# Optimization experiments

Measured on AMD Instinct MI355X. Metric: run time of the kernel, lower is better.

Reference implementation:

```python
import jax, jax.numpy as jnp
import numpy as np

INV_L_MIN, INV_L_MAX = 0.5, 2.0

def _gelu(v):
    return jax.nn.gelu(v, approximate=False)  # torch F.gelu default = exact erf

def compute_gradient(f, directed_edges, edge_gradient_weights):
    # f: [b, c, n] ; directed_edges: [b, e, 2] (target, source) ; egw: [b, e, d]
    f = jnp.transpose(f, (0, 2, 1))                      # [b, n, c]
    b, n, c = f.shape
    e, d = edge_gradient_weights.shape[1], edge_gradient_weights.shape[2]
    target, source = directed_edges[..., 0], directed_edges[..., 1]
    fs = jnp.take_along_axis(f, source[:, :, None], axis=1)   # [b, e, c]
    ft = jnp.take_along_axis(f, target[:, :, None], axis=1)   # [b, e, c]
    # einsum('bed,bec->becd') then reshape -> channel-major (c*d) layout
    msg = (edge_gradient_weights[:, :, None, :] * (fs - ft)[:, :, :, None]).reshape(b, e, c * d)
    seg = (target + n * jnp.arange(b, dtype=target.dtype)[:, None]).reshape(-1)
    grad = jax.ops.segment_sum(msg.reshape(b * e, c * d), seg, num_segments=b * n)
    return jnp.transpose(grad.reshape(b, n, c * d), (0, 2, 1))  # [b, c*d, n]

def spectral_conv(x, wc, ws_, w0, bc, bs, b0, wbc, wbs, wb0):
    # x: [b, c, n]; bases: [b, n, k, w]; weights: [c, o, k, w]
    xc = jnp.einsum('bcx,bxkw->bckw', x, wbc)
    xs = jnp.einsum('bcx,bxkw->bckw', x, wbs)
    x0 = jnp.einsum('bcx,bxkw->bckw', x, wb0)
    fc = jnp.einsum('bckw,cokw->bokw', xc, wc) - jnp.einsum('bckw,cokw->bokw', xs, ws_)
    fs = jnp.einsum('bckw,cokw->bokw', xs, wc) + jnp.einsum('bckw,cokw->bokw', xc, ws_)
    f0 = jnp.einsum('bckw,cokw->bokw', x0, w0)
    return (jnp.einsum('bokw,bxkw->box', f0, b0)
            + 2 * jnp.einsum('bokw,bxkw->box', fc, bc)
            - 2 * jnp.einsum('bokw,bxkw->box', fs, bs))

def setup_inputs():
    key = jax.random.key(0)
    ks = jax.random.split(key, 16)
    B, N, E = 4, 20000, 100000
    NDIMS, NMEAS, NMODES = 3, 1, 32
    C, L = 128, 3
    IN_DIM, FC_DIM, OUT_DIM = 3, 128, 1
    f32 = jnp.float32
    inp = {}
    inp['x'] = jax.random.normal(ks[0], (B, N, IN_DIM), f32)
    inp['node_mask'] = jnp.ones((B, N, 1), jnp.int32)
    inp['nodes'] = jax.random.uniform(ks[1], (B, N, NDIMS), f32)
    inp['node_weights'] = jax.random.uniform(ks[2], (B, N, NMEAS), f32) / N
    inp['directed_edges'] = jax.random.randint(ks[3], (B, E, 2), 0, N, jnp.int32)
    inp['edge_gradient_weights'] = jax.random.normal(ks[4], (B, E, NDIMS), f32)
    # modes k = 2*pi*K/L0, K integer-like
    inp['modes'] = (2 * jnp.pi * jax.random.randint(ks[5], (NMODES, NDIMS, NMEAS), 1, 9)).astype(f32)
    # scaled_logit(1.0, 0.5, 2.0): sigmoid(l)=1/3 -> l=log(0.5)
    inp['inv_L_scale_latent'] = jnp.full((NDIMS, NMEAS), np.log(0.5), f32)
    inp['fc0_w'] = jax.random.normal(ks[6], (C, IN_DIM), f32) / np.sqrt(IN_DIM)
    inp['fc0_b'] = jnp.zeros((C,), f32)
    sc = 1.0 / (C * C)
    inp['swc'] = sc * jax.random.uniform(ks[7], (L, C, C, NMODES, NMEAS), f32)
    inp['sws'] = sc * jax.random.uniform(ks[8], (L, C, C, NMODES, NMEAS), f32)
    inp['sw0'] = sc * jax.random.uniform(ks[9], (L, C, C, 1, NMEAS), f32)
    inp['ww'] = jax.random.normal(ks[10], (L, C, C), f32) / np.sqrt(C)
    inp['wb'] = jnp.zeros((L, C), f32)
    inp['gw'] = jax.random.normal(ks[11], (L, C, NDIMS * C), f32) / np.sqrt(NDIMS * C)
    inp['gb'] = jnp.zeros((L, C), f32)
    inp['fc1_w'] = jax.random.normal(ks[12], (FC_DIM, C), f32) / np.sqrt(C)
    inp['fc1_b'] = jnp.zeros((FC_DIM,), f32)
    inp['fc2_w'] = jax.random.normal(ks[13], (OUT_DIM, FC_DIM), f32) / np.sqrt(FC_DIM)
    inp['fc2_b'] = jnp.zeros((OUT_DIM,), f32)
    return inp

def reference(x, node_mask, nodes, node_weights, directed_edges, edge_gradient_weights,
              modes, inv_L_scale_latent, fc0_w, fc0_b, swc, sws, sw0, ww, wb, gw, gb,
              fc1_w, fc1_b, fc2_w, fc2_b):
    inv_L = INV_L_MIN + (INV_L_MAX - INV_L_MIN) * jax.nn.sigmoid(inv_L_scale_latent)  # [d, w]
    t = jnp.einsum('bxd,kdw->bxkw', nodes, modes * inv_L[None])
    bc, bs = jnp.cos(t), jnp.sin(t)
    b0 = jnp.ones(t.shape[:2] + (1, t.shape[3]), t.dtype)
    w = node_weights[:, :, None, :]
    wbc, wbs, wb0 = bc * w, bs * w, b0 * w
    h = jnp.einsum('bni,ci->bnc', x, fc0_w) + fc0_b        # lift
    h = jnp.transpose(h, (0, 2, 1))                        # [b, C, n]
    L = swc.shape[0]
    for i in range(L):
        h1 = spectral_conv(h, swc[i], sws[i], sw0[i], bc, bs, b0, wbc, wbs, wb0)
        h2 = jnp.einsum('oc,bcn->bon', ww[i], h) + wb[i][None, :, None]
        g = compute_gradient(h, directed_edges, edge_gradient_weights)
        h3 = jnp.einsum('oc,bcn->bon', gw[i], g) + gb[i][None, :, None]
        h = h1 + h2 + h3
        if i != L - 1:
            h = _gelu(h)
    h = jnp.transpose(h, (0, 2, 1))                        # [b, n, C]
    h = _gelu(h @ fc1_w.T + fc1_b)
    return h @ fc2_w.T + fc2_b                             # [b, n, out_dim]
```

## Files before the change

kernel.cpp:

```cpp
#include <hip/hip_runtime.h>
#include <math.h>

#define B_ 4
#define N_ 20000
#define E_ 100000
#define C_ 128
#define K_ 32
#define NPAD 20480
#define NROWS (B_*N_ + 128)

typedef __attribute__((ext_vector_type(8))) short short8;
typedef __attribute__((ext_vector_type(4))) float floatx4;
typedef __attribute__((ext_vector_type(4))) unsigned int uintx4;
typedef __attribute__((ext_vector_type(2))) unsigned int uintx2;

__device__ __forceinline__ float gelu_exact(float x){
    return 0.5f * x * (1.0f + erff(x * 0.70710678118654752f));
}

__device__ __forceinline__ unsigned short f2bf(float f){
    unsigned int u = __builtin_bit_cast(unsigned int, f);
    u += 0x7FFFu + ((u >> 16) & 1u);
    return (unsigned short)(u >> 16);
}
__device__ __forceinline__ unsigned int pack2(float a, float b){
    return (unsigned int)f2bf(a) | ((unsigned int)f2bf(b) << 16);
}
__device__ __forceinline__ float bf2f(unsigned short u){
    unsigned int v = ((unsigned int)u) << 16;
    return __builtin_bit_cast(float, v);
}
__device__ __forceinline__ float u2f(unsigned int u){
    return __builtin_bit_cast(float, u);
}


__global__ __launch_bounds__(256) void basis_kernel(
    const float* __restrict__ nodes, const float* __restrict__ nw,
    const float* __restrict__ modes, const float* __restrict__ latent,
    unsigned short* __restrict__ bcb, unsigned short* __restrict__ bsb,
    unsigned short* __restrict__ wBt)
{
    __shared__ float lx[64], ly[64], lz[64], lwv[64];
    __shared__ unsigned short lTc[32*64], lTs[32*64];
    int b = blockIdx.y, n0 = blockIdx.x*64;
    int tid = threadIdx.x;
    size_t bN = (size_t)b*N_;
    if (tid < 64){
        int n = n0 + tid;
        float iL0 = 0.5f + 1.5f/(1.f+expf(-latent[0]));
        float iL1 = 0.5f + 1.5f/(1.f+expf(-latent[1]));
        float iL2 = 0.5f + 1.5f/(1.f+expf(-latent[2]));
        if (n < N_){
            lx[tid] = nodes[(bN+n)*3+0]*iL0;
            ly[tid] = nodes[(bN+n)*3+1]*iL1;
            lz[tid] = nodes[(bN+n)*3+2]*iL2;
            lwv[tid] = nw[bN+n];
        } else { lx[tid]=0.f; ly[tid]=0.f; lz[tid]=0.f; lwv[tid]=0.f; }
    }
    __syncthreads();
    int node = tid>>2, k0 = (tid&3)*8;
    float p0 = lx[node], p1 = ly[node], p2 = lz[node], w = lwv[node];
    float cv[8], sv[8];
    #pragma unroll
    for (int i=0;i<8;i++){
        int k = k0+i;
        float t = p0*modes[k*3+0] + p1*modes[k*3+1] + p2*modes[k*3+2];
        cv[i] = cosf(t); sv[i] = sinf(t);
        lTc[k*64 + node] = f2bf(w*cv[i]);
        lTs[k*64 + node] = f2bf(w*sv[i]);
    }
    int gn = n0 + node;
    if (gn < N_){
        uintx4 uc = (uintx4){pack2(cv[0],cv[1]), pack2(cv[2],cv[3]),
                             pack2(cv[4],cv[5]), pack2(cv[6],cv[7])};
        uintx4 us = (uintx4){pack2(sv[0],sv[1]), pack2(sv[2],sv[3]),
                             pack2(sv[4],sv[5]), pack2(sv[6],sv[7])};
        *(uintx4*)&bcb[(bN+gn)*K_ + k0] = uc;
        *(uintx4*)&bsb[(bN+gn)*K_ + k0] = us;
    }
    __syncthreads();
    #pragma unroll
    for (int i=0;i<5;i++){
        int idx = i*256 + tid;
        int row = idx>>4, seg = idx&15;
        unsigned short v0,v1,v2,v3;
        if (row < 32){
            v0=lTc[row*64+seg*4+0]; v1=lTc[row*64+seg*4+1];
            v2=lTc[row*64+seg*4+2]; v3=lTc[row*64+seg*4+3];
        } else if (row < 64){
            int r = row-32;
            v0=lTs[r*64+seg*4+0]; v1=lTs[r*64+seg*4+1];
            v2=lTs[r*64+seg*4+2]; v3=lTs[r*64+seg*4+3];
        } else if (row == 64){
            v0=f2bf(lwv[seg*4+0]); v1=f2bf(lwv[seg*4+1]);
            v2=f2bf(lwv[seg*4+2]); v3=f2bf(lwv[seg*4+3]);
        } else { v0=v1=v2=v3=0; }
        uintx2 u;
        u.x = (unsigned int)v0 | ((unsigned int)v1<<16);
        u.y = (unsigned int)v2 | ((unsigned int)v3<<16);
        *(uintx2*)&wBt[((size_t)b*80+row)*NPAD + n0 + seg*4] = u;
    }
}


__global__ __launch_bounds__(256) void fc0_kernel(
    const float* __restrict__ x, const float* __restrict__ w,
    const float* __restrict__ bvec, unsigned short* __restrict__ hN,
    unsigned short* __restrict__ hT)
{
    int idx = blockIdx.x*256 + threadIdx.x;
    if (idx >= B_*N_) return;
    int b = idx / N_, n = idx - b*N_;
    float x0 = x[(size_t)idx*3+0], x1 = x[(size_t)idx*3+1], x2 = x[(size_t)idx*3+2];
    unsigned short* hr = hN + (size_t)idx*C_;
    for (int c=0;c<C_;c+=4){
        float4 v;
        v.x = bvec[c+0] + x0*w[(c+0)*3] + x1*w[(c+0)*3+1] + x2*w[(c+0)*3+2];
        v.y = bvec[c+1] + x0*w[(c+1)*3] + x1*w[(c+1)*3+1] + x2*w[(c+1)*3+2];
        v.z = bvec[c+2] + x0*w[(c+2)*3] + x1*w[(c+2)*3+1] + x2*w[(c+2)*3+2];
        v.w = bvec[c+3] + x0*w[(c+3)*3] + x1*w[(c+3)*3+1] + x2*w[(c+3)*3+2];
        uintx2 u; u.x = pack2(v.x,v.y); u.y = pack2(v.z,v.w);
        *(uintx2*)(hr+c) = u;
        hT[((size_t)b*C_+c+0)*NPAD + n] = f2bf(v.x);
        hT[((size_t)b*C_+c+1)*NPAD + n] = f2bf(v.y);
        hT[((size_t)b*C_+c+2)*NPAD + n] = f2bf(v.z);
        hT[((size_t)b*C_+c+3)*NPAD + n] = f2bf(v.w);
    }
}


__global__ __launch_bounds__(256) void hist_kernel(
    const int* __restrict__ edges, int* __restrict__ cnt)
{
    int idx = blockIdx.x*256 + threadIdx.x;
    if (idx >= B_*E_) return;
    int b = idx / E_;
    int t = edges[(size_t)idx*2];
    atomicAdd(cnt + b*N_ + t, 1);
}

__global__ __launch_bounds__(1024) void scan_kernel(
    const int* __restrict__ cnt, int* __restrict__ rowptr, int* __restrict__ cur)
{
    __shared__ int wsum[16];
    int b = blockIdx.x, tid = threadIdx.x;
    int lane = tid & 63, wv = tid >> 6;
    const int CHUNK = 20;
    int start = tid * CHUNK;
    int lc[CHUNK];
    int lsum = 0;
    #pragma unroll
    for (int i=0;i<CHUNK;i++){
        int n = start + i;
        int v = (n < N_) ? cnt[b*N_+n] : 0;
        lc[i] = v; lsum += v;
    }
    int v = lsum;
    #pragma unroll
    for (int off=1; off<64; off<<=1){
        int t = __shfl_up(v, off, 64);
        if (lane >= off) v += t;
    }
    if (lane == 63) wsum[wv] = v;
    __syncthreads();
    if (wv == 0 && lane < 16){
        int wv2 = wsum[lane];
        #pragma unroll
        for (int off=1; off<16; off<<=1){
            int t = __shfl_up(wv2, off, 64);
            if (lane >= off) wv2 += t;
        }
        wsum[lane] = wv2;
    }
    __syncthreads();
    int waveoff = (wv == 0) ? 0 : wsum[wv-1];
    int excl = waveoff + v - lsum;
    #pragma unroll
    for (int i=0;i<CHUNK;i++){
        int n = start + i;
        if (n < N_){
            rowptr[b*(N_+1)+n] = excl;
            cur[b*N_+n] = excl;
            excl += lc[i];
        }
    }
    if (tid == 0) rowptr[b*(N_+1)+N_] = E_;
}

__global__ __launch_bounds__(256) void fill_kernel(
    const int* __restrict__ edges, const float* __restrict__ egw,
    int* __restrict__ cur, uintx4* __restrict__ epack)
{
    int idx = blockIdx.x*256 + threadIdx.x;
    if (idx >= B_*E_) return;
    int b = idx / E_;
    int t = edges[(size_t)idx*2];
    int src = edges[(size_t)idx*2+1];
    uintx4 rec;
    rec.x = (unsigned int)src;
    rec.y = __builtin_bit_cast(unsigned int, egw[(size_t)idx*3+0]);
    rec.z = __builtin_bit_cast(unsigned int, egw[(size_t)idx*3+1]);
    rec.w = __builtin_bit_cast(unsigned int, egw[(size_t)idx*3+2]);
    int pos = atomicAdd(cur + b*N_ + t, 1);
    epack[(size_t)b*E_ + pos] = rec;
}


__global__ __launch_bounds__(256) void wconv_kernel(
    const float* __restrict__ ww, const float* __restrict__ gw,
    unsigned short* __restrict__ wcat3)
{
    int o = blockIdx.x, l = blockIdx.y, t = threadIdx.x;
    const float* ww_l = ww + (size_t)l*C_*C_;
    const float* gw_l = gw + (size_t)l*C_*C_*3;
    int k = t*2;
    float a, bv;
    if (k < 128){ a = ww_l[(size_t)o*C_ + k];      bv = ww_l[(size_t)o*C_ + k + 1]; }
    else        { a = gw_l[(size_t)o*384 + k-128]; bv = gw_l[(size_t)o*384 + k-127]; }
    *(unsigned int*)&wcat3[((size_t)l*C_ + o)*512 + k] = pack2(a, bv);
}

__global__ __launch_bounds__(64) void fc1conv_kernel(
    const float* __restrict__ fc1w, unsigned short* __restrict__ w16)
{
    int o = blockIdx.x, t = threadIdx.x;
    int k = t*2;
    *(unsigned int*)&w16[(size_t)o*C_ + k] = pack2(fc1w[(size_t)o*C_+k], fc1w[(size_t)o*C_+k+1]);
}


__global__ __launch_bounds__(256) void stageA_kernel(
    const unsigned short* __restrict__ hT, const unsigned short* __restrict__ wBt,
    float* __restrict__ part)
{
    __shared__ unsigned short As[80*72];
    __shared__ unsigned short Bs[128*72];
    int b = blockIdx.y, blk = blockIdx.x;
    int tid = threadIdx.x;
    int wv = tid>>6, lane = tid&63, l15 = lane&15, quad = lane>>4;
    floatx4 acc[5][2];
    #pragma unroll
    for (int mt=0;mt<5;mt++){ acc[mt][0]=(floatx4){0,0,0,0}; acc[mt][1]=(floatx4){0,0,0,0}; }
    size_t hbase = (size_t)b*C_*NPAD;
    size_t wbase = (size_t)b*80*NPAD;
    for (int cidx=0; cidx<5; ++cidx){
        int n0c = blk*320 + cidx*64;
        #pragma unroll
        for (int i=0;i<3;i++){
            int idx = i*256 + tid;
            if (idx < 640){
                int row = idx>>3, seg = idx&7;
                uintx4 v = *(const uintx4*)&wBt[wbase + (size_t)row*NPAD + n0c + seg*8];
                *(uintx4*)&As[row*72 + seg*8] = v;
            }
        }
        #pragma unroll
        for (int i=0;i<4;i++){
            int idx = i*256 + tid;
            int row = idx>>3, seg = idx&7;
            int node = n0c + seg*8;
            uintx4 v = (uintx4){0,0,0,0};
            if (node < N_)
                v = *(const uintx4*)&hT[hbase + (size_t)row*NPAD + node];
            *(uintx4*)&Bs[row*72 + seg*8] = v;
        }
        __syncthreads();
        #pragma unroll
        for (int ks=0; ks<2; ks++){
            short8 bfrag[2];
            #pragma unroll
            for (int ot=0;ot<2;ot++)
                bfrag[ot] = *(const short8*)&Bs[(wv*32+ot*16+l15)*72 + ks*32 + quad*8];
            #pragma unroll
            for (int mt=0;mt<5;mt++){
                short8 af = *(const short8*)&As[(mt*16+l15)*72 + ks*32 + quad*8];
                acc[mt][0] = __builtin_amdgcn_mfma_f32_16x16x32_bf16(af, bfrag[0], acc[mt][0], 0,0,0);
                acc[mt][1] = __builtin_amdgcn_mfma_f32_16x16x32_bf16(af, bfrag[1], acc[mt][1], 0,0,0);
            }
        }
        __syncthreads();
    }
    float* pblk = part + ((size_t)(b*64+blk))*80*C_;
    #pragma unroll
    for (int mt=0;mt<5;mt++){
        #pragma unroll
        for (int ot=0;ot<2;ot++){
            int c = wv*32 + ot*16 + l15;
            #pragma unroll
            for (int r=0;r<4;r++){
                int kcol = mt*16 + quad*4 + r;
                pblk[kcol*C_ + c] = acc[mt][ot][r];
            }
        }
    }
}

__global__ __launch_bounds__(256) void reducePart_kernel(
    const float* __restrict__ part, float* __restrict__ xq)
{
    int idx = blockIdx.x*256 + threadIdx.x;
    if (idx >= B_*80*C_) return;
    int b = idx / (80*C_);
    int r = idx - b*80*C_;
    float s = 0.f;
    for (int blk=0; blk<64; blk++)
        s += part[((size_t)(b*64+blk))*80*C_ + r];
    xq[idx] = s;
}


__global__ __launch_bounds__(256) void mix_kernel(
    const float* __restrict__ xq, const float* __restrict__ swc_l,
    const float* __restrict__ sws_l, const float* __restrict__ sw0_l,
    unsigned short* __restrict__ wfb, float* __restrict__ f0)
{
    __shared__ float s64[4][64];
    int o = blockIdx.x, tid = threadIdx.x;
    int b = tid >> 6, t = tid & 63;
    int k = t & 31; bool isS = t >= 32;
    const float* xqb = xq + (size_t)b*80*C_;
    float acc = 0.f;
    for (int c=0;c<C_;c++){
        float xc = xqb[k*C_ + c], xs = xqb[(32+k)*C_ + c];
        float wc = swc_l[((size_t)c*C_+o)*K_ + k];
        float ws = sws_l[((size_t)c*C_+o)*K_ + k];
        acc += isS ? (xs*wc + xc*ws) : (xc*wc - xs*ws);
    }
    wfb[((size_t)b*C_+o)*64 + t] = f2bf(isS ? -2.f*acc : 2.f*acc);
    float p = xqb[64*C_ + t]      * sw0_l[(size_t)t*C_+o]
            + xqb[64*C_ + 64 + t] * sw0_l[(size_t)(t+64)*C_+o];
    s64[b][t] = p; __syncthreads();
    if (t==0){
        float s=0.f;
        for (int i=0;i<64;i++) s += s64[b][i];
        f0[b*C_+o] = s;
    }
}


__global__ __launch_bounds__(256) void grad_kernel(
    const unsigned short* __restrict__ hN, const uintx4* __restrict__ epack,
    const int* __restrict__ rowptr, unsigned short* __restrict__ g)
{
    int flat = blockIdx.x;
    int xcd = flat & 7;
    int b = xcd >> 1;
    int grp = (flat >> 3)*2 + (xcd & 1);
    int n = grp*4 + (threadIdx.x >> 6);
    int cp = threadIdx.x & 63;
    size_t bN = (size_t)b*N_;
    size_t bE = (size_t)b*E_;
    int r0 = rowptr[b*(N_+1)+n], r1 = rowptr[b*(N_+1)+n+1];
    unsigned int hcu = *(const unsigned int*)&hN[(bN+n)*C_ + cp*2];
    float hc0 = bf2f((unsigned short)hcu), hc1 = bf2f((unsigned short)(hcu>>16));
    float a00=0.f,a01=0.f,a02=0.f, a10=0.f,a11=0.f,a12=0.f;
    int i = r0;
    for (; i + 1 < r1; i += 2){
        uintx4 p0 = epack[bE + i];
        uintx4 p1 = epack[bE + i + 1];
        int s0 = (int)p0.x, s1 = (int)p1.x;
        unsigned int u0 = *(const unsigned int*)&hN[(bN+s0)*C_ + cp*2];
        unsigned int u1 = *(const unsigned int*)&hN[(bN+s1)*C_ + cp*2];
        float w00 = u2f(p0.y), w01 = u2f(p0.z), w02 = u2f(p0.w);
        float w10 = u2f(p1.y), w11 = u2f(p1.z), w12 = u2f(p1.w);
        float d00 = bf2f((unsigned short)u0) - hc0;
        float d01 = bf2f((unsigned short)(u0>>16)) - hc1;
        float d10 = bf2f((unsigned short)u1) - hc0;
        float d11 = bf2f((unsigned short)(u1>>16)) - hc1;
        a00 += w00*d00; a01 += w01*d00; a02 += w02*d00;
        a10 += w00*d01; a11 += w01*d01; a12 += w02*d01;
        a00 += w10*d10; a01 += w11*d10; a02 += w12*d10;
        a10 += w10*d11; a11 += w11*d11; a12 += w12*d11;
    }
    if (i < r1){
        uintx4 p0 = epack[bE + i];
        int s0 = (int)p0.x;
        unsigned int u0 = *(const unsigned int*)&hN[(bN+s0)*C_ + cp*2];
        float w00 = u2f(p0.y), w01 = u2f(p0.z), w02 = u2f(p0.w);
        float d00 = bf2f((unsigned short)u0) - hc0;
        float d01 = bf2f((unsigned short)(u0>>16)) - hc1;
        a00 += w00*d00; a01 += w01*d00; a02 += w02*d00;
        a10 += w00*d01; a11 += w01*d01; a12 += w02*d01;
    }
    unsigned short* gr = g + (bN+n)*(size_t)384 + cp*6;
    *(unsigned int*)(gr+0) = pack2(a00,a01);
    *(unsigned int*)(gr+2) = pack2(a02,a10);
    *(unsigned int*)(gr+4) = pack2(a11,a12);
}


__global__ __launch_bounds__(256) void gemm_kernel(
    const unsigned short* __restrict__ hN, const unsigned short* __restrict__ g,
    const unsigned short* __restrict__ bcb, const unsigned short* __restrict__ bsb,
    const unsigned short* __restrict__ wcat, const unsigned short* __restrict__ wfb,
    const float* __restrict__ wb_l, const float* __restrict__ gb_l,
    const float* __restrict__ f0,
    unsigned short* __restrict__ hNo, unsigned short* __restrict__ hT, int apply_gelu)
{
    __shared__ unsigned short As[2][64*72];
    int b = blockIdx.y;
    int nb0 = blockIdx.x*64;
    int tid = threadIdx.x;
    int a_n = tid>>2, a_s = tid&3;
    int wv = tid>>6, lane = tid&63, l15 = lane&15, quad = lane>>4;
    floatx4 acc[4][2];
    #pragma unroll
    for (int mt=0;mt<4;mt++)
        #pragma unroll
        for (int ot=0;ot<2;ot++) acc[mt][ot] = (floatx4){0.f,0.f,0.f,0.f};
    size_t bN = (size_t)b*N_;
    int gn = nb0 + a_n; bool av = gn < N_;
    size_t row = bN + (size_t)(av ? gn : 0);
    const unsigned short* hrow  = hN + row*C_;
    const unsigned short* grow  = g  + row*384;
    const unsigned short* bcrow = bcb + row*K_;
    const unsigned short* bsrow = bsb + row*K_;
    int o0 = wv*32 + l15, o1 = o0 + 16;
    const unsigned short* w0p = wcat + (size_t)o0*512 + quad*8;
    const unsigned short* w1p = wcat + (size_t)o1*512 + quad*8;
    const unsigned short* fb0 = wfb + ((size_t)b*C_ + o0)*64 + quad*8;
    const unsigned short* fb1 = wfb + ((size_t)b*C_ + o1)*64 + quad*8;

    auto loadA = [&](int ch, uintx4& v0, uintx4& v1){
        v0 = (uintx4){0,0,0,0}; v1 = (uintx4){0,0,0,0};
        if (av){
            if (ch < 8){
                const uintx4* p = (ch<2) ? (const uintx4*)(hrow + ch*64 + a_s*16)
                                         : (const uintx4*)(grow + (ch-2)*64 + a_s*16);
                v0 = p[0]; v1 = p[1];
            } else {
                const uintx4* p = (a_s < 2) ? (const uintx4*)(bcrow + a_s*16)
                                            : (const uintx4*)(bsrow + (a_s-2)*16);
                v0 = p[0]; v1 = p[1];
            }
        }
    };

    uintx4 c0, c1;
    loadA(0, c0, c1);
    *(uintx4*)&As[0][a_n*72 + a_s*16]     = c0;
    *(uintx4*)&As[0][a_n*72 + a_s*16 + 8] = c1;
    int p = 0;
    for (int ch=0; ch<9; ++ch){
        uintx4 n0v, n1v;
        if (ch < 8) loadA(ch+1, n0v, n1v);
        __syncthreads();
        #pragma unroll
        for (int ks=0; ks<2; ks++){
            short8 bfr0, bfr1;
            if (ch < 8){
                bfr0 = *(const short8*)(w0p + ch*64 + ks*32);
                bfr1 = *(const short8*)(w1p + ch*64 + ks*32);
            } else {
                bfr0 = *(const short8*)(fb0 + ks*32);
                bfr1 = *(const short8*)(fb1 + ks*32);
            }
            #pragma unroll
            for (int mt=0; mt<4; mt++){
                short8 af = *(const short8*)&As[p][(mt*16+l15)*72 + ks*32 + quad*8];
                acc[mt][0] = __builtin_amdgcn_mfma_f32_16x16x32_bf16(af, bfr0, acc[mt][0], 0,0,0);
                acc[mt][1] = __builtin_amdgcn_mfma_f32_16x16x32_bf16(af, bfr1, acc[mt][1], 0,0,0);
            }
        }
        if (ch < 8){
            *(uintx4*)&As[1-p][a_n*72 + a_s*16]     = n0v;
            *(uintx4*)&As[1-p][a_n*72 + a_s*16 + 8] = n1v;
            p ^= 1;
        }
    }
    float biasv[2]; int oo[2];
    oo[0]=o0; oo[1]=o1;
    #pragma unroll
    for (int ot=0;ot<2;ot++)
        biasv[ot] = wb_l[oo[ot]] + gb_l[oo[ot]] + f0[(size_t)b*C_ + oo[ot]];
    unsigned short* AsF = &As[0][0];
    if (apply_gelu) __syncthreads();
    #pragma unroll
    for (int mt=0;mt<4;mt++){
        #pragma unroll
        for (int ot=0;ot<2;ot++){
            int nb = nb0 + mt*16 + quad*4;
            float v4[4];
            #pragma unroll
            for (int r=0;r<4;r++){
                float vv = acc[mt][ot][r] + biasv[ot];
                if (apply_gelu) vv = gelu_exact(vv);
                v4[r] = vv;
                if (nb + r < N_) hNo[(bN+nb+r)*C_ + oo[ot]] = f2bf(vv);
            }
            if (apply_gelu){
                uintx2 u; u.x = pack2(v4[0],v4[1]); u.y = pack2(v4[2],v4[3]);
                *(uintx2*)&AsF[oo[ot]*72 + mt*16 + quad*4] = u;
            }
        }
    }
    if (apply_gelu){
        __syncthreads();
        int orow = tid>>1, half = tid&1;
        uintx4 u0 = *(const uintx4*)&AsF[orow*72 + half*32];
        uintx4 u1 = *(const uintx4*)&AsF[orow*72 + half*32 + 8];
        unsigned short* dst = &hT[((size_t)b*C_ + orow)*NPAD + nb0 + half*32];
        *(uintx4*)dst       = u0;
        *(uintx4*)(dst + 8) = u1;
    }
}


__global__ __launch_bounds__(256) void final_kernel(
    const unsigned short* __restrict__ hN, const unsigned short* __restrict__ fc1b16,
    const float* __restrict__ fc1b, const float* __restrict__ fc2w,
    const float* __restrict__ fc2b, float* __restrict__ out)
{
    __shared__ unsigned short As[64*72];
    __shared__ float pp[4*64];
    int b = blockIdx.y;
    int nb0 = blockIdx.x*64;
    int tid = threadIdx.x;
    int a_n = tid>>2, a_s = tid&3;
    int wv = tid>>6, lane = tid&63, l15 = lane&15, quad = lane>>4;
    floatx4 acc[4][2];
    #pragma unroll
    for (int mt=0;mt<4;mt++){ acc[mt][0]=(floatx4){0,0,0,0}; acc[mt][1]=(floatx4){0,0,0,0}; }
    size_t bN = (size_t)b*N_;
    int gn = nb0 + a_n; bool av = gn < N_;
    size_t row = bN + (size_t)(av ? gn : 0);
    const unsigned short* hrow = hN + row*C_;
    int o0 = wv*32 + l15, o1 = o0 + 16;
    const unsigned short* w0p = fc1b16 + (size_t)o0*C_ + quad*8;
    const unsigned short* w1p = fc1b16 + (size_t)o1*C_ + quad*8;

    for (int ch=0; ch<2; ++ch){
        uintx4 v0 = (uintx4){0,0,0,0}, v1 = (uintx4){0,0,0,0};
        if (av){
            const uintx4* pptr = (const uintx4*)(hrow + ch*64 + a_s*16);
            v0 = pptr[0]; v1 = pptr[1];
        }
        *(uintx4*)&As[a_n*72 + a_s*16]     = v0;
        *(uintx4*)&As[a_n*72 + a_s*16 + 8] = v1;
        __syncthreads();
        #pragma unroll
        for (int ks=0; ks<2; ks++){
            short8 bfr0 = *(const short8*)(w0p + ch*64 + ks*32);
            short8 bfr1 = *(const short8*)(w1p + ch*64 + ks*32);
            #pragma unroll
            for (int mt=0; mt<4; mt++){
                short8 af = *(const short8*)&As[(mt*16+l15)*72 + ks*32 + quad*8];
                acc[mt][0] = __builtin_amdgcn_mfma_f32_16x16x32_bf16(af, bfr0, acc[mt][0], 0,0,0);
                acc[mt][1] = __builtin_amdgcn_mfma_f32_16x16x32_bf16(af, bfr1, acc[mt][1], 0,0,0);
            }
        }
        __syncthreads();
    }
    float fw0 = fc2w[o0], fw1 = fc2w[o1];
    float b0 = fc1b[o0], b1 = fc1b[o1];
    #pragma unroll
    for (int mt=0;mt<4;mt++){
        float s[4];
        #pragma unroll
        for (int r=0;r<4;r++)
            s[r] = fw0*gelu_exact(acc[mt][0][r] + b0) + fw1*gelu_exact(acc[mt][1][r] + b1);
        #pragma unroll
        for (int m=1;m<16;m<<=1)
            #pragma unroll
            for (int r=0;r<4;r++)
                s[r] += __shfl_xor(s[r], m, 16);
        if (l15 < 4){
            float v = (l15==0)?s[0]:(l15==1)?s[1]:(l15==2)?s[2]:s[3];
            pp[wv*64 + mt*16 + quad*4 + l15] = v;
        }
    }
    __syncthreads();
    if (tid < 64){
        float sum = pp[tid] + pp[64+tid] + pp[128+tid] + pp[192+tid] + fc2b[0];
        int n = nb0 + tid;
        if (n < N_) out[bN + n] = sum;
    }
}


extern "C" void kernel_launch(void* const* d_in, const int* in_sizes, int n_in,
                              void* d_out, int out_size, void* d_ws, size_t ws_size,
                              hipStream_t stream)
{
    const float* x      = (const float*)d_in[0];
    const float* nodes  = (const float*)d_in[2];
    const float* nw     = (const float*)d_in[3];
    const int*   edges  = (const int*)  d_in[4];
    const float* egw    = (const float*)d_in[5];
    const float* modes  = (const float*)d_in[6];
    const float* latent = (const float*)d_in[7];
    const float* fc0w   = (const float*)d_in[8];
    const float* fc0b   = (const float*)d_in[9];
    const float* swc    = (const float*)d_in[10];
    const float* sws    = (const float*)d_in[11];
    const float* sw0    = (const float*)d_in[12];
    const float* ww     = (const float*)d_in[13];
    const float* wb     = (const float*)d_in[14];
    const float* gw     = (const float*)d_in[15];
    const float* gb     = (const float*)d_in[16];
    const float* fc1w   = (const float*)d_in[17];
    const float* fc1b   = (const float*)d_in[18];
    const float* fc2w   = (const float*)d_in[19];
    const float* fc2b   = (const float*)d_in[20];
    float* out = (float*)d_out;

    char* W = (char*)d_ws;
    size_t off = 0;
    unsigned short* bcB = (unsigned short*)(W+off); off += (size_t)NROWS*K_*2;
    unsigned short* bsB = (unsigned short*)(W+off); off += (size_t)NROWS*K_*2;
    unsigned short* wBt = (unsigned short*)(W+off); off += (size_t)B_*80*NPAD*2;
    unsigned short* hT  = (unsigned short*)(W+off); off += (size_t)B_*C_*NPAD*2;
    unsigned short* hNa = (unsigned short*)(W+off); off += (size_t)NROWS*C_*2;
    unsigned short* hNb = (unsigned short*)(W+off); off += (size_t)NROWS*C_*2;
    unsigned short* g   = (unsigned short*)(W+off); off += (size_t)NROWS*C_*3*2;
    unsigned short* wcat3=(unsigned short*)(W+off); off += (size_t)3*C_*512*2;
    unsigned short* wfb = (unsigned short*)(W+off); off += (size_t)B_*C_*64*2;
    unsigned short* fcw16=(unsigned short*)(W+off); off += (size_t)C_*C_*2;
    float* part = (float*)(W+off); off += (size_t)B_*64*80*C_*4;
    float* xq   = (float*)(W+off); off += (size_t)B_*80*C_*4;
    float* f0   = (float*)(W+off); off += (size_t)B_*C_*4;
    off = (off + 15) & ~(size_t)15;
    uintx4* epack = (uintx4*)(W+off); off += (size_t)B_*E_*16;
    int* cnt    = (int*)(W+off); off += (size_t)B_*N_*4;
    int* rowptr = (int*)(W+off); off += (size_t)B_*(N_+1)*4 + 16;
    int* cur    = (int*)(W+off); off += (size_t)B_*N_*4;

    (void)hipMemsetAsync(cnt, 0, (size_t)B_*N_*sizeof(int), stream);
    basis_kernel<<<dim3(NPAD/64, B_), 256, 0, stream>>>(
        nodes, nw, modes, latent, bcB, bsB, wBt);
    fc0_kernel  <<<(B_*N_+255)/256, 256, 0, stream>>>(x, fc0w, fc0b, hNa, hT);
    hist_kernel <<<(B_*E_+255)/256, 256, 0, stream>>>(edges, cnt);
    scan_kernel <<<B_, 1024, 0, stream>>>(cnt, rowptr, cur);
    fill_kernel <<<(B_*E_+255)/256, 256, 0, stream>>>(edges, egw, cur, epack);
    wconv_kernel<<<dim3(C_,3), 256, 0, stream>>>(ww, gw, wcat3);
    fc1conv_kernel<<<C_, 64, 0, stream>>>(fc1w, fcw16);

    unsigned short* hc = hNa; unsigned short* hn = hNb;
    for (int l=0; l<3; ++l){
        stageA_kernel<<<dim3(64,B_), 256, 0, stream>>>(hT, wBt, part);
        reducePart_kernel<<<(B_*80*C_+255)/256, 256, 0, stream>>>(part, xq);
        mix_kernel<<<C_, 256, 0, stream>>>(
            xq, swc + (size_t)l*C_*C_*K_, sws + (size_t)l*C_*C_*K_,
            sw0 + (size_t)l*C_*C_, wfb, f0);
        grad_kernel<<<N_, 256, 0, stream>>>(hc, epack, rowptr, g);
        gemm_kernel<<<dim3((N_+63)/64,B_), 256, 0, stream>>>(
            hc, g, bcB, bsB, wcat3 + (size_t)l*C_*512, wfb,
            wb + (size_t)l*C_, gb + (size_t)l*C_,
            f0, hn, hT, (l<2) ? 1 : 0);
        unsigned short* t = hc; hc = hn; hn = t;
    }
    final_kernel<<<dim3((N_+63)/64,B_), 256, 0, stream>>>(
        hc, fcw16, fc1b, fc2w, fc2b, out);
}
```

Baseline: 576.4 us.

## Replace partial-sum reduction with atomics and deepen gemm K-stages

The stageA kernel now accumulates its per-block partial spectral coefficients directly into xq with float atomicAdd after a memset, removing the separate reducePart kernel and its partial buffer. The gemm kernel's A-tile staging is widened from 64 to 128 K-elements per stage (5 stages instead of 9), which halves the number of barriers and buffer swaps at the cost of more LDS and registers per block. Atomics add contention across 64 blocks per batch and make the summation order nondeterministic.

```diff
diff --git a/kernel.cpp b/kernel.cpp
--- a/kernel.cpp
+++ b/kernel.cpp
@@ -232,7 +232,7 @@
 
 __global__ __launch_bounds__(256) void stageA_kernel(
     const unsigned short* __restrict__ hT, const unsigned short* __restrict__ wBt,
-    float* __restrict__ part)
+    float* __restrict__ xq)
 {
     __shared__ unsigned short As[80*72];
     __shared__ unsigned short Bs[128*72];
@@ -281,7 +281,7 @@
         }
         __syncthreads();
     }
-    float* pblk = part + ((size_t)(b*64+blk))*80*C_;
+    float* xqb = xq + (size_t)b*80*C_;
     #pragma unroll
     for (int mt=0;mt<5;mt++){
         #pragma unroll
@@ -290,23 +290,10 @@
             #pragma unroll
             for (int r=0;r<4;r++){
                 int kcol = mt*16 + quad*4 + r;
-                pblk[kcol*C_ + c] = acc[mt][ot][r];
-            }
-        }
-    }
-}
-
-__global__ __launch_bounds__(256) void reducePart_kernel(
-    const float* __restrict__ part, float* __restrict__ xq)
-{
-    int idx = blockIdx.x*256 + threadIdx.x;
-    if (idx >= B_*80*C_) return;
-    int b = idx / (80*C_);
-    int r = idx - b*80*C_;
-    float s = 0.f;
-    for (int blk=0; blk<64; blk++)
-        s += part[((size_t)(b*64+blk))*80*C_ + r];
-    xq[idx] = s;
+                atomicAdd(&xqb[kcol*C_ + c], acc[mt][ot][r]);
+            }
+        }
+    }
 }
 
 
@@ -398,7 +385,7 @@
     const float* __restrict__ f0,
     unsigned short* __restrict__ hNo, unsigned short* __restrict__ hT, int apply_gelu)
 {
-    __shared__ unsigned short As[2][64*72];
+    __shared__ unsigned short As[2][64*136];
     int b = blockIdx.y;
     int nb0 = blockIdx.x*64;
     int tid = threadIdx.x;
@@ -422,51 +409,67 @@
     const unsigned short* fb0 = wfb + ((size_t)b*C_ + o0)*64 + quad*8;
     const unsigned short* fb1 = wfb + ((size_t)b*C_ + o1)*64 + quad*8;
 
-    auto loadA = [&](int ch, uintx4& v0, uintx4& v1){
-        v0 = (uintx4){0,0,0,0}; v1 = (uintx4){0,0,0,0};
+    auto loadStage = [&](int s, uintx4 v[4]){
+        v[0]=(uintx4){0,0,0,0}; v[1]=(uintx4){0,0,0,0};
+        v[2]=(uintx4){0,0,0,0}; v[3]=(uintx4){0,0,0,0};
         if (av){
-            if (ch < 8){
-                const uintx4* p = (ch<2) ? (const uintx4*)(hrow + ch*64 + a_s*16)
-                                         : (const uintx4*)(grow + (ch-2)*64 + a_s*16);
-                v0 = p[0]; v1 = p[1];
+            if (s < 4){
+                const uintx4* p = (s==0) ? (const uintx4*)(hrow + a_s*32)
+                                         : (const uintx4*)(grow + (s-1)*128 + a_s*32);
+                v[0]=p[0]; v[1]=p[1]; v[2]=p[2]; v[3]=p[3];
             } else {
                 const uintx4* p = (a_s < 2) ? (const uintx4*)(bcrow + a_s*16)
                                             : (const uintx4*)(bsrow + (a_s-2)*16);
-                v0 = p[0]; v1 = p[1];
+                v[0]=p[0]; v[1]=p[1];
             }
         }
     };
-
-    uintx4 c0, c1;
-    loadA(0, c0, c1);
-    *(uintx4*)&As[0][a_n*72 + a_s*16]     = c0;
-    *(uintx4*)&As[0][a_n*72 + a_s*16 + 8] = c1;
+    auto storeStage = [&](int s, uintx4 v[4], int buf){
+        if (s < 4){
+            #pragma unroll
+            for (int j=0;j<4;j++)
+                *(uintx4*)&As[buf][a_n*136 + a_s*32 + j*8] = v[j];
+        } else {
+            *(uintx4*)&As[buf][a_n*136 + a_s*16]     = v[0];
+            *(uintx4*)&As[buf][a_n*136 + a_s*16 + 8] = v[1];
+        }
+    };
+
+    uintx4 cur[4];
+    loadStage(0, cur);
+    storeStage(0, cur, 0);
     int p = 0;
-    for (int ch=0; ch<9; ++ch){
-        uintx4 n0v, n1v;
-        if (ch < 8) loadA(ch+1, n0v, n1v);
+    for (int s=0; s<5; ++s){
+        uintx4 nxt[4];
+        if (s < 4) loadStage(s+1, nxt);
         __syncthreads();
-        #pragma unroll
-        for (int ks=0; ks<2; ks++){
-            short8 bfr0, bfr1;
-            if (ch < 8){
-                bfr0 = *(const short8*)(w0p + ch*64 + ks*32);
-                bfr1 = *(const short8*)(w1p + ch*64 + ks*32);
-            } else {
-                bfr0 = *(const short8*)(fb0 + ks*32);
-                bfr1 = *(const short8*)(fb1 + ks*32);
-            }
-            #pragma unroll
-            for (int mt=0; mt<4; mt++){
-                short8 af = *(const short8*)&As[p][(mt*16+l15)*72 + ks*32 + quad*8];
-                acc[mt][0] = __builtin_amdgcn_mfma_f32_16x16x32_bf16(af, bfr0, acc[mt][0], 0,0,0);
-                acc[mt][1] = __builtin_amdgcn_mfma_f32_16x16x32_bf16(af, bfr1, acc[mt][1], 0,0,0);
-            }
-        }
-        if (ch < 8){
-            *(uintx4*)&As[1-p][a_n*72 + a_s*16]     = n0v;
-            *(uintx4*)&As[1-p][a_n*72 + a_s*16 + 8] = n1v;
+        if (s < 4){
+            #pragma unroll
+            for (int ksl=0; ksl<4; ksl++){
+                int ksg = s*4 + ksl;
+                short8 bfr0 = *(const short8*)(w0p + ksg*32);
+                short8 bfr1 = *(const short8*)(w1p + ksg*32);
+                #pragma unroll
+                for (int mt=0; mt<4; mt++){
+                    short8 af = *(const short8*)&As[p][(mt*16+l15)*136 + ksl*32 + quad*8];
+                    acc[mt][0] = __builtin_amdgcn_mfma_f32_16x16x32_bf16(af, bfr0, acc[mt][0], 0,0,0);
+                    acc[mt][1] = __builtin_amdgcn_mfma_f32_16x16x32_bf16(af, bfr1, acc[mt][1], 0,0,0);
+                }
+            }
+            storeStage(s+1, nxt, 1-p);
             p ^= 1;
+        } else {
+            #pragma unroll
+            for (int ksl=0; ksl<2; ksl++){
+                short8 bfr0 = *(const short8*)(fb0 + ksl*32);
+                short8 bfr1 = *(const short8*)(fb1 + ksl*32);
+                #pragma unroll
+                for (int mt=0; mt<4; mt++){
+                    short8 af = *(const short8*)&As[p][(mt*16+l15)*136 + ksl*32 + quad*8];
+                    acc[mt][0] = __builtin_amdgcn_mfma_f32_16x16x32_bf16(af, bfr0, acc[mt][0], 0,0,0);
+                    acc[mt][1] = __builtin_amdgcn_mfma_f32_16x16x32_bf16(af, bfr1, acc[mt][1], 0,0,0);
+                }
+            }
         }
     }
     float biasv[2]; int oo[2];
@@ -617,7 +620,6 @@
     unsigned short* wcat3=(unsigned short*)(W+off); off += (size_t)3*C_*512*2;
     unsigned short* wfb = (unsigned short*)(W+off); off += (size_t)B_*C_*64*2;
     unsigned short* fcw16=(unsigned short*)(W+off); off += (size_t)C_*C_*2;
-    float* part = (float*)(W+off); off += (size_t)B_*64*80*C_*4;
     float* xq   = (float*)(W+off); off += (size_t)B_*80*C_*4;
     float* f0   = (float*)(W+off); off += (size_t)B_*C_*4;
     off = (off + 15) & ~(size_t)15;
@@ -638,8 +640,8 @@
 
     unsigned short* hc = hNa; unsigned short* hn = hNb;
     for (int l=0; l<3; ++l){
-        stageA_kernel<<<dim3(64,B_), 256, 0, stream>>>(hT, wBt, part);
-        reducePart_kernel<<<(B_*80*C_+255)/256, 256, 0, stream>>>(part, xq);
+        (void)hipMemsetAsync(xq, 0, (size_t)B_*80*C_*4, stream);
+        stageA_kernel<<<dim3(64,B_), 256, 0, stream>>>(hT, wBt, xq);
         mix_kernel<<<C_, 256, 0, stream>>>(
             xq, swc + (size_t)l*C_*C_*K_, sws + (size_t)l*C_*C_*K_,
             sw0 + (size_t)l*C_*C_, wfb, f0);
```

New measurement: 587.0 us. Within noise of the previous version (+1.8%).
